# Kernel tuning notes

Measured on AMD Instinct MI355X. Metric: run time of the kernel, lower is better.

The kernel has to match this reference:

```python
import jax, jax.numpy as jnp
import numpy as np

H, I, QKV, TV = 2048, 8192, 8192, 4096
NVH, NKH, KD, VD, KC = 32, 16, 128, 128, 4

def _rms(x, w, eps=1e-6):
    # [x,-x]->LayerNorm trick: doubled mean is 0, so it reduces to x*rsqrt(mean(x^2)+eps)
    return x * jax.lax.rsqrt(jnp.mean(x * x, -1, keepdims=True) + eps) * (1.0 + w)

def _silu(x):
    return x * jax.nn.sigmoid(x)

def setup_inputs() -> dict:
    key = jax.random.key(0)
    ks = jax.random.split(key, 16)
    w = lambda i, shape, s=0.02: jax.random.normal(ks[i], shape, jnp.float32) * s
    return {
        'x': jax.random.normal(ks[0], (1, H), jnp.float32),
        'conv_state': jax.random.normal(ks[1], (QKV, KC), jnp.float32) * 0.1,
        'ssm_state': jax.random.normal(ks[2], (NVH, KD, VD), jnp.float32) * 0.1,
        'in_proj_w': w(3, (QKV + TV + 2 * NVH, H)),
        'out_proj_w': w(4, (H, TV)),
        'conv_weight': w(5, (QKV, KC), 0.5),
        'A_log': w(6, (NVH,), 0.1),
        'dt_bias': w(7, (NVH,), 0.1),
        'norm_weight': jnp.ones((VD,), jnp.float32),
        'rms1_w': w(8, (H,)),
        'rms2_w': w(9, (H,)),
        'gate_w': w(10, (I, H)),
        'up_w': w(11, (I, H)),
        'down_w': w(12, (H, I)),
    }

def reference(x, conv_state, ssm_state, in_proj_w, out_proj_w, conv_weight,
              A_log, dt_bias, norm_weight, rms1_w, rms2_w, gate_w, up_w, down_w):
    residual = x  # [1, H]
    h = _rms(x, rms1_w)
    proj = h @ in_proj_w.T  # [1, QKV+TV+2*NVH]
    mixed_qkv = proj[:, :QKV]
    z = proj[:, QKV:QKV + TV]
    a_raw = proj[0, QKV + TV:QKV + TV + NVH]
    b_raw = proj[0, QKV + TV + NVH:]

    # causal conv step: shift state, append new token, depthwise conv + silu
    new_conv_state = jnp.concatenate([conv_state[:, 1:], mixed_qkv[0][:, None]], axis=1)  # [QKV, KC]
    conv_out = _silu(jnp.sum(new_conv_state * conv_weight, axis=1))  # [QKV]

    KT = NKH * KD
    q = conv_out[:KT].reshape(NKH, KD)
    k = conv_out[KT:2 * KT].reshape(NKH, KD)
    v = conv_out[2 * KT:].reshape(NVH, VD)
    ratio = NVH // NKH
    q = jnp.repeat(q, ratio, axis=0)  # [NVH, KD]
    k = jnp.repeat(k, ratio, axis=0)
    l2 = lambda t: t / jnp.maximum(jnp.linalg.norm(t, axis=-1, keepdims=True), 1e-12)
    q = l2(q) * (KD ** -0.5)
    k = l2(k)

    beta = jax.nn.sigmoid(b_raw)  # [NVH]
    g = -jnp.exp(A_log) * jax.nn.softplus(a_raw + dt_bias)
    decay = jnp.exp(g)  # [NVH]

    # delta-rule fast-weight update
    decayed = decay[:, None, None] * ssm_state  # [NVH, KD, VD]
    Sk = jnp.einsum('hkv,hk->hv', decayed, k)
    delta = (v - Sk) * beta[:, None]
    new_ssm = decayed + k[:, :, None] * delta[:, None, :]
    y = jnp.einsum('hkv,hk->hv', new_ssm, q)  # [NVH, VD]

    # doubled-LayerNorm (eps=1e-6) with direct weight (not 1+w)
    y_n = y * jax.lax.rsqrt(jnp.mean(y * y, -1, keepdims=True) + 1e-6) * norm_weight
    y_out = (y_n * _silu(z.reshape(NVH, VD))).reshape(1, -1)  # [1, TV]
    attn_out = y_out @ out_proj_w.T
    x1 = residual + attn_out

    h2 = _rms(x1, rms2_w)
    ffn = (_silu(h2 @ gate_w.T) * (h2 @ up_w.T)) @ down_w.T
    return (x1 + ffn, new_conv_state, new_ssm)
```

## Files before the change

### kernel.cpp

```cpp
#include <hip/hip_runtime.h>
#include <math.h>

#define HD    2048
#define QKVD  8192
#define TVD   4096
#define NVHD  32
#define NKHD  16
#define KDD   128
#define VDD   128
#define PROJN (QKVD + TVD + 2*NVHD)

typedef float f4 __attribute__((ext_vector_type(4)));

__device__ __forceinline__ float sigmoidf_(float x) { return 1.0f / (1.0f + expf(-x)); }
__device__ __forceinline__ float siluf_(float x)    { return x / (1.0f + expf(-x)); }
__device__ __forceinline__ float softplusf_(float x){ return (x > 20.0f) ? x : log1pf(expf(x)); }
__device__ __forceinline__ float dot4(f4 a, f4 b)   { return a.x*b.x + a.y*b.y + a.z*b.z + a.w*b.w; }
__device__ __forceinline__ f4 ntload(const f4* p)   { return __builtin_nontemporal_load(p); }

__device__ __forceinline__ float waveReduceSum(float v) {
#pragma unroll
    for (int o = 32; o > 0; o >>= 1) v += __shfl_down(v, o, 64);
    return v;
}

template<int NW>
__device__ __forceinline__ float blockReduceSum(float v, float* red) {
    const int lane = threadIdx.x & 63, wid = threadIdx.x >> 6;
    v = waveReduceSum(v);
    if (lane == 0) red[wid] = v;
    __syncthreads();
    float s = 0.f;
#pragma unroll
    for (int w = 0; w < NW; w++) s += red[w];
    __syncthreads();
    return s;
}

__global__ void kA_inproj(const float* __restrict__ x, const float* __restrict__ w1,
                          const float* __restrict__ W, float* __restrict__ proj) {
    __shared__ float red[4];
    __shared__ float hl[HD];
    const int t = threadIdx.x;

    f4 xv[2];
    float s = 0.f;
#pragma unroll
    for (int i = 0; i < 2; i++) {
        xv[i] = ((const f4*)x)[t + i*256];
        s += dot4(xv[i], xv[i]);
    }
    s = blockReduceSum<4>(s, red);
    const float r = rsqrtf(s / (float)HD + 1e-6f);
#pragma unroll
    for (int i = 0; i < 2; i++) {
        f4 wv = ((const f4*)w1)[t + i*256];
        ((f4*)hl)[t + i*256] = xv[i] * r * (wv + 1.0f);
    }
    __syncthreads();

    const int wid = t >> 6, lane = t & 63;
    const int row = blockIdx.x * 4 + wid;
    const f4* Wr = (const f4*)(W + (size_t)row * HD);
    float acc = 0.f;
#pragma unroll
    for (int i = 0; i < 8; i++) {
        f4 a = ntload(&Wr[lane + i*64]);
        f4 b = ((const f4*)hl)[lane + i*64];
        acc += dot4(a, b);
    }
    acc = waveReduceSum(acc);
    if (lane == 0) proj[row] = acc;
}

__global__ void kB_ssm(const float* __restrict__ proj,
                       const float* __restrict__ conv_state,
                       const float* __restrict__ conv_weight,
                       const float* __restrict__ ssm_state,
                       const float* __restrict__ A_log,
                       const float* __restrict__ dt_bias,
                       const float* __restrict__ norm_weight,
                       float* __restrict__ new_conv_state,
                       float* __restrict__ new_ssm,
                       float* __restrict__ yout) {
    const int head  = blockIdx.x;
    const int t     = threadIdx.x;
    const int qhead = head >> 1;

    __shared__ float red[8];
    __shared__ float q_s[KDD], k_s[KDD], v_s[VDD];
    __shared__ float skr2[512], sqr2[512];

    float qv = 0.f, kv = 0.f, vv = 0.f;
    if (t < 128) {
        int cq = qhead*KDD + t;
        f4 cs = *(const f4*)(conv_state + (size_t)cq*4);
        f4 w  = *(const f4*)(conv_weight + (size_t)cq*4);
        float xm = proj[cq];
        qv = siluf_(cs.y*w.x + cs.z*w.y + cs.w*w.z + xm*w.w);
        f4 nc; nc.x = cs.y; nc.y = cs.z; nc.z = cs.w; nc.w = xm;
        *(f4*)(new_conv_state + (size_t)cq*4) = nc;

        int ck = 2048 + qhead*KDD + t;
        cs = *(const f4*)(conv_state + (size_t)ck*4);
        w  = *(const f4*)(conv_weight + (size_t)ck*4);
        xm = proj[ck];
        kv = siluf_(cs.y*w.x + cs.z*w.y + cs.w*w.z + xm*w.w);
        nc.x = cs.y; nc.y = cs.z; nc.z = cs.w; nc.w = xm;
        *(f4*)(new_conv_state + (size_t)ck*4) = nc;

        int cv = 4096 + head*VDD + t;
        cs = *(const f4*)(conv_state + (size_t)cv*4);
        w  = *(const f4*)(conv_weight + (size_t)cv*4);
        xm = proj[cv];
        vv = siluf_(cs.y*w.x + cs.z*w.y + cs.w*w.z + xm*w.w);
        nc.x = cs.y; nc.y = cs.z; nc.z = cs.w; nc.w = xm;
        *(f4*)(new_conv_state + (size_t)cv*4) = nc;
    }

    const float sq = blockReduceSum<8>(qv*qv, red);
    const float sk = blockReduceSum<8>(kv*kv, red);
    const float qn = qv / fmaxf(sqrtf(sq), 1e-12f) * 0.08838834764831845f;
    const float kn = kv / fmaxf(sqrtf(sk), 1e-12f);
    const float kq = blockReduceSum<8>(qn*kn, red);

    if (t < 128) { q_s[t] = qn; k_s[t] = kn; v_s[t] = vv; }
    __syncthreads();

    const float a_raw = proj[QKVD + TVD + head];
    const float b_raw = proj[QKVD + TVD + NVHD + head];
    const float beta  = sigmoidf_(b_raw);
    const float g     = -expf(A_log[head]) * softplusf_(a_raw + dt_bias[head]);
    const float decay = expf(g);

    const int col = t & 127;
    const int kh  = t >> 7;
    const float* Sp = ssm_state + (size_t)head*KDD*VDD + (size_t)kh*32*VDD + col;
    float skr = 0.f, sqr = 0.f;
#pragma unroll 8
    for (int k = 0; k < 32; k++) {
        float sv = Sp[k*VDD];
        skr += sv * k_s[kh*32 + k];
        sqr += sv * q_s[kh*32 + k];
    }
    skr2[t] = skr; sqr2[t] = sqr;
    __syncthreads();
    const float Skr = skr2[col] + skr2[col+128] + skr2[col+256] + skr2[col+384];
    const float Sqr = sqr2[col] + sqr2[col+128] + sqr2[col+256] + sqr2[col+384];
    const float delta = (v_s[col] - decay * Skr) * beta;

    float* Np = new_ssm + (size_t)head*KDD*VDD + (size_t)kh*32*VDD + col;
#pragma unroll 8
    for (int k = 0; k < 32; k++) {
        float sv = Sp[k*VDD];
        Np[k*VDD] = decay * sv + k_s[kh*32 + k] * delta;
    }

    const float y = decay * Sqr + delta * kq;
    const float sy = blockReduceSum<8>((kh == 0) ? y*y : 0.f, red);
    if (t < 128) {
        const float rr = rsqrtf(sy / (float)VDD + 1e-6f);
        const float z  = proj[QKVD + head*VDD + t];
        yout[head*VDD + t] = y * rr * norm_weight[t] * siluf_(z);
    }
}

__global__ void kC_outproj(const float* __restrict__ W, const float* __restrict__ y,
                           const float* __restrict__ x, float* __restrict__ x1) {
    __shared__ float part[4];
    const int t = threadIdx.x, wid = t >> 6, lane = t & 63;
    const int row = blockIdx.x;
    const f4* Wr = (const f4*)(W + (size_t)row * TVD);
    const f4* vr = (const f4*)y;
    float acc = 0.f;
#pragma unroll
    for (int i = 0; i < 4; i++) {
        int idx = wid*256 + i*64 + lane;
        acc += dot4(ntload(&Wr[idx]), vr[idx]);
    }
    acc = waveReduceSum(acc);
    if (lane == 0) part[wid] = acc;
    __syncthreads();
    if (t == 0) x1[row] = x[row] + part[0] + part[1] + part[2] + part[3];
}

__global__ void kD_gateup(const float* __restrict__ GW, const float* __restrict__ UW,
                          const float* __restrict__ x1, const float* __restrict__ w2,
                          float* __restrict__ m) {
    __shared__ float red[4];
    __shared__ float tl[HD];
    const int t = threadIdx.x;

    f4 xv[2];
    float s = 0.f;
#pragma unroll
    for (int i = 0; i < 2; i++) {
        xv[i] = ((const f4*)x1)[t + i*256];
        s += dot4(xv[i], xv[i]);
    }
    s = blockReduceSum<4>(s, red);
    const float r = rsqrtf(s / (float)HD + 1e-6f);
#pragma unroll
    for (int i = 0; i < 2; i++) {
        f4 wv = ((const f4*)w2)[t + i*256];
        ((f4*)tl)[t + i*256] = xv[i] * (wv + 1.0f);
    }
    __syncthreads();

    const int wid = t >> 6, lane = t & 63;
    const int row = blockIdx.x * 4 + wid;
    const f4* Gr = (const f4*)(GW + (size_t)row * HD);
    const f4* Ur = (const f4*)(UW + (size_t)row * HD);
    float ag = 0.f, au = 0.f;
#pragma unroll
    for (int i = 0; i < 8; i++) {
        f4 tt = ((const f4*)tl)[lane + i*64];
        ag += dot4(ntload(&Gr[lane + i*64]), tt);
        au += dot4(ntload(&Ur[lane + i*64]), tt);
    }
    ag = waveReduceSum(ag);
    au = waveReduceSum(au);
    if (lane == 0) {
        ag *= r; au *= r;
        m[row] = siluf_(ag) * au;
    }
}

__global__ void kE_down(const float* __restrict__ W, const float* __restrict__ m,
                        const float* __restrict__ x1, float* __restrict__ out0) {
    __shared__ float part[4];
    const int t = threadIdx.x, wid = t >> 6, lane = t & 63;
    const int row = blockIdx.x;
    const f4* Wr = (const f4*)(W + (size_t)row * 8192);
    const f4* vr = (const f4*)m;
    float acc = 0.f;
#pragma unroll
    for (int i = 0; i < 8; i++) {
        int idx = wid*512 + i*64 + lane;
        acc += dot4(ntload(&Wr[idx]), vr[idx]);
    }
    acc = waveReduceSum(acc);
    if (lane == 0) part[wid] = acc;
    __syncthreads();
    if (t == 0) out0[row] = x1[row] + part[0] + part[1] + part[2] + part[3];
}

extern "C" void kernel_launch(void* const* d_in, const int* in_sizes, int n_in,
                              void* d_out, int out_size, void* d_ws, size_t ws_size,
                              hipStream_t stream) {
    const float* x           = (const float*)d_in[0];
    const float* conv_state  = (const float*)d_in[1];
    const float* ssm_state   = (const float*)d_in[2];
    const float* in_proj_w   = (const float*)d_in[3];
    const float* out_proj_w  = (const float*)d_in[4];
    const float* conv_weight = (const float*)d_in[5];
    const float* A_log       = (const float*)d_in[6];
    const float* dt_bias     = (const float*)d_in[7];
    const float* norm_weight = (const float*)d_in[8];
    const float* rms1_w      = (const float*)d_in[9];
    const float* rms2_w      = (const float*)d_in[10];
    const float* gate_w      = (const float*)d_in[11];
    const float* up_w        = (const float*)d_in[12];
    const float* down_w      = (const float*)d_in[13];

    float* out0     = (float*)d_out;
    float* new_conv = out0 + HD;
    float* new_ssm  = new_conv + QKVD*4;

    float* ws   = (float*)d_ws;
    float* proj = ws;
    float* yout = proj + PROJN;
    float* x1   = yout + TVD;
    float* mmid = x1 + HD;

    kA_inproj<<<PROJN/4, 256, 0, stream>>>(x, rms1_w, in_proj_w, proj);
    kB_ssm<<<NVHD, 512, 0, stream>>>(proj, conv_state, conv_weight, ssm_state,
                                     A_log, dt_bias, norm_weight,
                                     new_conv, new_ssm, yout);
    kC_outproj<<<HD, 256, 0, stream>>>(out_proj_w, yout, x, x1);
    kD_gateup<<<8192/4, 256, 0, stream>>>(gate_w, up_w, x1, rms2_w, mmid);
    kE_down<<<HD, 256, 0, stream>>>(down_w, mmid, x1, out0);
}
```

Before: 311.3 us.

## Remove shared-memory staging and block syncs from GEMV kernels; one row per wave

The in-projection and gate/up kernels now have each wave compute the RMS-norm scale and the normalized input vector in registers, instead of staging them in shared memory behind block-wide barriers. The RMS scale is applied to the final dot product rather than to the input. The out-proj and down-proj kernels switch from four waves sharing one row (shared-memory partial sums plus a barrier) to one row per wave, with a quarter as many blocks. This drops barriers and LDS traffic, but the small input vector is now re-read per wave and each wave streams a longer row.

```diff
diff --git a/kernel.cpp b/kernel.cpp
--- a/kernel.cpp
+++ b/kernel.cpp
@@ -5,7 +5,6 @@
 #define QKVD  8192
 #define TVD   4096
 #define NVHD  32
-#define NKHD  16
 #define KDD   128
 #define VDD   128
 #define PROJN (QKVD + TVD + 2*NVHD)
@@ -39,38 +38,26 @@
 
 __global__ void kA_inproj(const float* __restrict__ x, const float* __restrict__ w1,
                           const float* __restrict__ W, float* __restrict__ proj) {
-    __shared__ float red[4];
-    __shared__ float hl[HD];
-    const int t = threadIdx.x;
-
-    f4 xv[2];
-    float s = 0.f;
-#pragma unroll
-    for (int i = 0; i < 2; i++) {
-        xv[i] = ((const f4*)x)[t + i*256];
-        s += dot4(xv[i], xv[i]);
-    }
-    s = blockReduceSum<4>(s, red);
-    const float r = rsqrtf(s / (float)HD + 1e-6f);
-#pragma unroll
-    for (int i = 0; i < 2; i++) {
-        f4 wv = ((const f4*)w1)[t + i*256];
-        ((f4*)hl)[t + i*256] = xv[i] * r * (wv + 1.0f);
-    }
-    __syncthreads();
-
-    const int wid = t >> 6, lane = t & 63;
-    const int row = blockIdx.x * 4 + wid;
+    const int t = threadIdx.x, wid = t >> 6, lane = t & 63;
+    const int row = blockIdx.x * 4 + wid;
+
+    f4 tt[8];
+    float ss = 0.f;
+#pragma unroll
+    for (int i = 0; i < 8; i++) {
+        f4 xv = ((const f4*)x)[lane + i*64];
+        f4 wv = ((const f4*)w1)[lane + i*64];
+        ss += dot4(xv, xv);
+        tt[i] = xv * (wv + 1.0f);
+    }
     const f4* Wr = (const f4*)(W + (size_t)row * HD);
     float acc = 0.f;
 #pragma unroll
-    for (int i = 0; i < 8; i++) {
-        f4 a = ntload(&Wr[lane + i*64]);
-        f4 b = ((const f4*)hl)[lane + i*64];
-        acc += dot4(a, b);
-    }
+    for (int i = 0; i < 8; i++)
+        acc += dot4(ntload(&Wr[lane + i*64]), tt[i]);
     acc = waveReduceSum(acc);
-    if (lane == 0) proj[row] = acc;
+    ss  = waveReduceSum(ss);
+    if (lane == 0) proj[row] = acc * rsqrtf(ss / (float)HD + 1e-6f);
 }
 
 __global__ void kB_ssm(const float* __restrict__ proj,
@@ -167,82 +154,62 @@
 
 __global__ void kC_outproj(const float* __restrict__ W, const float* __restrict__ y,
                            const float* __restrict__ x, float* __restrict__ x1) {
-    __shared__ float part[4];
-    const int t = threadIdx.x, wid = t >> 6, lane = t & 63;
-    const int row = blockIdx.x;
+    const int t = threadIdx.x, wid = t >> 6, lane = t & 63;
+    const int row = blockIdx.x * 4 + wid;
     const f4* Wr = (const f4*)(W + (size_t)row * TVD);
     const f4* vr = (const f4*)y;
     float acc = 0.f;
-#pragma unroll
-    for (int i = 0; i < 4; i++) {
-        int idx = wid*256 + i*64 + lane;
-        acc += dot4(ntload(&Wr[idx]), vr[idx]);
-    }
+#pragma unroll 8
+    for (int i = 0; i < 16; i++)
+        acc += dot4(ntload(&Wr[lane + i*64]), vr[lane + i*64]);
     acc = waveReduceSum(acc);
-    if (lane == 0) part[wid] = acc;
-    __syncthreads();
-    if (t == 0) x1[row] = x[row] + part[0] + part[1] + part[2] + part[3];
+    if (lane == 0) x1[row] = x[row] + acc;
 }
 
 __global__ void kD_gateup(const float* __restrict__ GW, const float* __restrict__ UW,
                           const float* __restrict__ x1, const float* __restrict__ w2,
                           float* __restrict__ m) {
-    __shared__ float red[4];
-    __shared__ float tl[HD];
-    const int t = threadIdx.x;
-
-    f4 xv[2];
-    float s = 0.f;
-#pragma unroll
-    for (int i = 0; i < 2; i++) {
-        xv[i] = ((const f4*)x1)[t + i*256];
-        s += dot4(xv[i], xv[i]);
-    }
-    s = blockReduceSum<4>(s, red);
-    const float r = rsqrtf(s / (float)HD + 1e-6f);
-#pragma unroll
-    for (int i = 0; i < 2; i++) {
-        f4 wv = ((const f4*)w2)[t + i*256];
-        ((f4*)tl)[t + i*256] = xv[i] * (wv + 1.0f);
-    }
-    __syncthreads();
-
-    const int wid = t >> 6, lane = t & 63;
-    const int row = blockIdx.x * 4 + wid;
+    const int t = threadIdx.x, wid = t >> 6, lane = t & 63;
+    const int row = blockIdx.x * 4 + wid;
+
+    f4 tt[8];
+    float ss = 0.f;
+#pragma unroll
+    for (int i = 0; i < 8; i++) {
+        f4 xv = ((const f4*)x1)[lane + i*64];
+        f4 wv = ((const f4*)w2)[lane + i*64];
+        ss += dot4(xv, xv);
+        tt[i] = xv * (wv + 1.0f);
+    }
     const f4* Gr = (const f4*)(GW + (size_t)row * HD);
     const f4* Ur = (const f4*)(UW + (size_t)row * HD);
     float ag = 0.f, au = 0.f;
-#pragma unroll
+#pragma unroll 4
     for (int i = 0; i < 8; i++) {
-        f4 tt = ((const f4*)tl)[lane + i*64];
-        ag += dot4(ntload(&Gr[lane + i*64]), tt);
-        au += dot4(ntload(&Ur[lane + i*64]), tt);
+        ag += dot4(ntload(&Gr[lane + i*64]), tt[i]);
+        au += dot4(ntload(&Ur[lane + i*64]), tt[i]);
     }
     ag = waveReduceSum(ag);
     au = waveReduceSum(au);
+    ss = waveReduceSum(ss);
     if (lane == 0) {
-        ag *= r; au *= r;
-        m[row] = siluf_(ag) * au;
+        const float r = rsqrtf(ss / (float)HD + 1e-6f);
+        m[row] = siluf_(ag * r) * (au * r);
     }
 }
 
 __global__ void kE_down(const float* __restrict__ W, const float* __restrict__ m,
                         const float* __restrict__ x1, float* __restrict__ out0) {
-    __shared__ float part[4];
-    const int t = threadIdx.x, wid = t >> 6, lane = t & 63;
-    const int row = blockIdx.x;
+    const int t = threadIdx.x, wid = t >> 6, lane = t & 63;
+    const int row = blockIdx.x * 4 + wid;
     const f4* Wr = (const f4*)(W + (size_t)row * 8192);
     const f4* vr = (const f4*)m;
     float acc = 0.f;
-#pragma unroll
-    for (int i = 0; i < 8; i++) {
-        int idx = wid*512 + i*64 + lane;
-        acc += dot4(ntload(&Wr[idx]), vr[idx]);
-    }
+#pragma unroll 8
+    for (int i = 0; i < 32; i++)
+        acc += dot4(ntload(&Wr[lane + i*64]), vr[lane + i*64]);
     acc = waveReduceSum(acc);
-    if (lane == 0) part[wid] = acc;
-    __syncthreads();
-    if (t == 0) out0[row] = x1[row] + part[0] + part[1] + part[2] + part[3];
+    if (lane == 0) out0[row] = x1[row] + acc;
 }
 
 extern "C" void kernel_launch(void* const* d_in, const int* in_sizes, int n_in,
@@ -277,7 +244,7 @@
     kB_ssm<<<NVHD, 512, 0, stream>>>(proj, conv_state, conv_weight, ssm_state,
                                      A_log, dt_bias, norm_weight,
                                      new_conv, new_ssm, yout);
-    kC_outproj<<<HD, 256, 0, stream>>>(out_proj_w, yout, x, x1);
+    kC_outproj<<<HD/4, 256, 0, stream>>>(out_proj_w, yout, x, x1);
     kD_gateup<<<8192/4, 256, 0, stream>>>(gate_w, up_w, x1, rms2_w, mmid);
-    kE_down<<<HD, 256, 0, stream>>>(down_w, mmid, x1, out0);
-}
+    kE_down<<<HD/4, 256, 0, stream>>>(down_w, mmid, x1, out0);
+}
```

Measured after the change: 322.8 us. +3.7%, slower.

## Fuse all stages into one persistent kernel with grid barriers

Applied to the files above, without the earlier changes.

Replaces the five separate kernel launches with one persistent 128-block kernel that moves between stages through atomic grid barriers, removing launch gaps and tail idle time. While 32 blocks run the SSM head update, the other blocks pre-read the out-projection weights to warm the cache for the next stage. The out-projection now uses cached loads instead of nontemporal ones. The risks are fewer blocks in flight to saturate HBM bandwidth for the large GEMVs, barrier spin overhead, and a hang if all 128 blocks are not co-resident.

```diff
diff --git a/kernel.cpp b/kernel.cpp
--- a/kernel.cpp
+++ b/kernel.cpp
@@ -5,10 +5,11 @@
 #define QKVD  8192
 #define TVD   4096
 #define NVHD  32
-#define NKHD  16
 #define KDD   128
 #define VDD   128
 #define PROJN (QKVD + TVD + 2*NVHD)
+#define NB    128
+#define BT    256
 
 typedef float f4 __attribute__((ext_vector_type(4)));
 
@@ -37,212 +38,220 @@
     return s;
 }
 
-__global__ void kA_inproj(const float* __restrict__ x, const float* __restrict__ w1,
-                          const float* __restrict__ W, float* __restrict__ proj) {
+__device__ __forceinline__ void gridBar(int* bar, int idx) {
+    __syncthreads();
+    __threadfence();
+    if (threadIdx.x == 0) {
+        __hip_atomic_fetch_add(&bar[idx], 1, __ATOMIC_ACQ_REL, __HIP_MEMORY_SCOPE_AGENT);
+        while (__hip_atomic_load(&bar[idx], __ATOMIC_ACQUIRE, __HIP_MEMORY_SCOPE_AGENT) < NB)
+            __builtin_amdgcn_s_sleep(8);
+    }
+    __syncthreads();
+    __threadfence();
+}
+
+__global__ void init_bar(int* bar) {
+    if (threadIdx.x < 8) bar[threadIdx.x] = 0;
+}
+
+__global__ __launch_bounds__(BT)
+void mega(const float* __restrict__ x, const float* __restrict__ conv_state,
+          const float* __restrict__ ssm_state, const float* __restrict__ in_proj_w,
+          const float* __restrict__ out_proj_w, const float* __restrict__ conv_weight,
+          const float* __restrict__ A_log, const float* __restrict__ dt_bias,
+          const float* __restrict__ norm_weight, const float* __restrict__ rms1_w,
+          const float* __restrict__ rms2_w, const float* __restrict__ gate_w,
+          const float* __restrict__ up_w, const float* __restrict__ down_w,
+          float* __restrict__ out0, float* __restrict__ new_conv,
+          float* __restrict__ new_ssm, float* __restrict__ proj,
+          float* __restrict__ yout, float* __restrict__ x1, float* __restrict__ mmid,
+          int* __restrict__ bar) {
+    __shared__ float hl[HD];
     __shared__ float red[4];
-    __shared__ float hl[HD];
-    const int t = threadIdx.x;
-
-    f4 xv[2];
-    float s = 0.f;
-#pragma unroll
-    for (int i = 0; i < 2; i++) {
-        xv[i] = ((const f4*)x)[t + i*256];
-        s += dot4(xv[i], xv[i]);
-    }
-    s = blockReduceSum<4>(s, red);
-    const float r = rsqrtf(s / (float)HD + 1e-6f);
-#pragma unroll
-    for (int i = 0; i < 2; i++) {
-        f4 wv = ((const f4*)w1)[t + i*256];
-        ((f4*)hl)[t + i*256] = xv[i] * r * (wv + 1.0f);
-    }
-    __syncthreads();
-
+    __shared__ float q_s[KDD], k_s[KDD], v_s[VDD];
+    __shared__ float skr2[256], sqr2[256];
+    const int t = threadIdx.x, bid = blockIdx.x;
     const int wid = t >> 6, lane = t & 63;
-    const int row = blockIdx.x * 4 + wid;
-    const f4* Wr = (const f4*)(W + (size_t)row * HD);
-    float acc = 0.f;
-#pragma unroll
-    for (int i = 0; i < 8; i++) {
-        f4 a = ntload(&Wr[lane + i*64]);
-        f4 b = ((const f4*)hl)[lane + i*64];
-        acc += dot4(a, b);
-    }
-    acc = waveReduceSum(acc);
-    if (lane == 0) proj[row] = acc;
-}
-
-__global__ void kB_ssm(const float* __restrict__ proj,
-                       const float* __restrict__ conv_state,
-                       const float* __restrict__ conv_weight,
-                       const float* __restrict__ ssm_state,
-                       const float* __restrict__ A_log,
-                       const float* __restrict__ dt_bias,
-                       const float* __restrict__ norm_weight,
-                       float* __restrict__ new_conv_state,
-                       float* __restrict__ new_ssm,
-                       float* __restrict__ yout) {
-    const int head  = blockIdx.x;
-    const int t     = threadIdx.x;
-    const int qhead = head >> 1;
-
-    __shared__ float red[8];
-    __shared__ float q_s[KDD], k_s[KDD], v_s[VDD];
-    __shared__ float skr2[512], sqr2[512];
-
-    float qv = 0.f, kv = 0.f, vv = 0.f;
-    if (t < 128) {
-        int cq = qhead*KDD + t;
-        f4 cs = *(const f4*)(conv_state + (size_t)cq*4);
-        f4 w  = *(const f4*)(conv_weight + (size_t)cq*4);
-        float xm = proj[cq];
-        qv = siluf_(cs.y*w.x + cs.z*w.y + cs.w*w.z + xm*w.w);
-        f4 nc; nc.x = cs.y; nc.y = cs.z; nc.z = cs.w; nc.w = xm;
-        *(f4*)(new_conv_state + (size_t)cq*4) = nc;
-
-        int ck = 2048 + qhead*KDD + t;
-        cs = *(const f4*)(conv_state + (size_t)ck*4);
-        w  = *(const f4*)(conv_weight + (size_t)ck*4);
-        xm = proj[ck];
-        kv = siluf_(cs.y*w.x + cs.z*w.y + cs.w*w.z + xm*w.w);
-        nc.x = cs.y; nc.y = cs.z; nc.z = cs.w; nc.w = xm;
-        *(f4*)(new_conv_state + (size_t)ck*4) = nc;
-
-        int cv = 4096 + head*VDD + t;
-        cs = *(const f4*)(conv_state + (size_t)cv*4);
-        w  = *(const f4*)(conv_weight + (size_t)cv*4);
-        xm = proj[cv];
-        vv = siluf_(cs.y*w.x + cs.z*w.y + cs.w*w.z + xm*w.w);
-        nc.x = cs.y; nc.y = cs.z; nc.z = cs.w; nc.w = xm;
-        *(f4*)(new_conv_state + (size_t)cv*4) = nc;
-    }
-
-    const float sq = blockReduceSum<8>(qv*qv, red);
-    const float sk = blockReduceSum<8>(kv*kv, red);
-    const float qn = qv / fmaxf(sqrtf(sq), 1e-12f) * 0.08838834764831845f;
-    const float kn = kv / fmaxf(sqrtf(sk), 1e-12f);
-    const float kq = blockReduceSum<8>(qn*kn, red);
-
-    if (t < 128) { q_s[t] = qn; k_s[t] = kn; v_s[t] = vv; }
-    __syncthreads();
-
-    const float a_raw = proj[QKVD + TVD + head];
-    const float b_raw = proj[QKVD + TVD + NVHD + head];
-    const float beta  = sigmoidf_(b_raw);
-    const float g     = -expf(A_log[head]) * softplusf_(a_raw + dt_bias[head]);
-    const float decay = expf(g);
-
-    const int col = t & 127;
-    const int kh  = t >> 7;
-    const float* Sp = ssm_state + (size_t)head*KDD*VDD + (size_t)kh*32*VDD + col;
-    float skr = 0.f, sqr = 0.f;
+
+    {
+        f4 xv[2];
+        float s = 0.f;
+#pragma unroll
+        for (int i = 0; i < 2; i++) {
+            xv[i] = ((const f4*)x)[t + i*256];
+            s += dot4(xv[i], xv[i]);
+        }
+        s = blockReduceSum<4>(s, red);
+        const float r = rsqrtf(s / (float)HD + 1e-6f);
+#pragma unroll
+        for (int i = 0; i < 2; i++) {
+            f4 wv = ((const f4*)rms1_w)[t + i*256];
+            ((f4*)hl)[t + i*256] = xv[i] * r * (wv + 1.0f);
+        }
+        __syncthreads();
+    }
+
+    for (int row = bid*4 + wid; row < PROJN; row += NB*4) {
+        const f4* Wr = (const f4*)(in_proj_w + (size_t)row * HD);
+        float acc = 0.f;
+#pragma unroll
+        for (int i = 0; i < 8; i++)
+            acc += dot4(ntload(&Wr[lane + i*64]), ((const f4*)hl)[lane + i*64]);
+        acc = waveReduceSum(acc);
+        if (lane == 0) proj[row] = acc;
+    }
+    gridBar(bar, 0);
+
+    if (bid < NVHD) {
+        const int head = bid, qhead = head >> 1;
+        float qv = 0.f, kv = 0.f, vv = 0.f;
+        if (t < 128) {
+            int cq = qhead*KDD + t;
+            f4 cs = *(const f4*)(conv_state + (size_t)cq*4);
+            f4 w  = *(const f4*)(conv_weight + (size_t)cq*4);
+            float xm = proj[cq];
+            qv = siluf_(cs.y*w.x + cs.z*w.y + cs.w*w.z + xm*w.w);
+            f4 nc; nc.x = cs.y; nc.y = cs.z; nc.z = cs.w; nc.w = xm;
+            *(f4*)(new_conv + (size_t)cq*4) = nc;
+
+            int ck = 2048 + qhead*KDD + t;
+            cs = *(const f4*)(conv_state + (size_t)ck*4);
+            w  = *(const f4*)(conv_weight + (size_t)ck*4);
+            xm = proj[ck];
+            kv = siluf_(cs.y*w.x + cs.z*w.y + cs.w*w.z + xm*w.w);
+            nc.x = cs.y; nc.y = cs.z; nc.z = cs.w; nc.w = xm;
+            *(f4*)(new_conv + (size_t)ck*4) = nc;
+
+            int cv = 4096 + head*VDD + t;
+            cs = *(const f4*)(conv_state + (size_t)cv*4);
+            w  = *(const f4*)(conv_weight + (size_t)cv*4);
+            xm = proj[cv];
+            vv = siluf_(cs.y*w.x + cs.z*w.y + cs.w*w.z + xm*w.w);
+            nc.x = cs.y; nc.y = cs.z; nc.z = cs.w; nc.w = xm;
+            *(f4*)(new_conv + (size_t)cv*4) = nc;
+        }
+
+        const float sq = blockReduceSum<4>(qv*qv, red);
+        const float sk = blockReduceSum<4>(kv*kv, red);
+        const float qn = qv / fmaxf(sqrtf(sq), 1e-12f) * 0.08838834764831845f;
+        const float kn = kv / fmaxf(sqrtf(sk), 1e-12f);
+        const float kq = blockReduceSum<4>(qn*kn, red);
+
+        if (t < 128) { q_s[t] = qn; k_s[t] = kn; v_s[t] = vv; }
+        __syncthreads();
+
+        const float a_raw = proj[QKVD + TVD + head];
+        const float b_raw = proj[QKVD + TVD + NVHD + head];
+        const float beta  = sigmoidf_(b_raw);
+        const float g     = -expf(A_log[head]) * softplusf_(a_raw + dt_bias[head]);
+        const float decay = expf(g);
+
+        const int col = t & 127;
+        const int kh  = t >> 7;
+        const float* Sp = ssm_state + (size_t)head*KDD*VDD + (size_t)kh*64*VDD + col;
+        float skr = 0.f, sqr = 0.f;
+#pragma unroll 16
+        for (int k = 0; k < 64; k++) {
+            float sv = Sp[k*VDD];
+            skr += sv * k_s[kh*64 + k];
+            sqr += sv * q_s[kh*64 + k];
+        }
+        skr2[t] = skr; sqr2[t] = sqr;
+        __syncthreads();
+        const float Skr = skr2[col] + skr2[col + 128];
+        const float Sqr = sqr2[col] + sqr2[col + 128];
+        const float delta = (v_s[col] - decay * Skr) * beta;
+
+        float* Np = new_ssm + (size_t)head*KDD*VDD + (size_t)kh*64*VDD + col;
+#pragma unroll 16
+        for (int k = 0; k < 64; k++) {
+            float sv = Sp[k*VDD];
+            Np[k*VDD] = decay * sv + k_s[kh*64 + k] * delta;
+        }
+
+        const float y = decay * Sqr + delta * kq;
+        const float sy = blockReduceSum<4>((kh == 0) ? y*y : 0.f, red);
+        if (t < 128) {
+            const float rr = rsqrtf(sy / (float)VDD + 1e-6f);
+            const float z  = proj[QKVD + head*VDD + t];
+            yout[head*VDD + t] = y * rr * norm_weight[t] * siluf_(z);
+        }
+    } else {
+        const f4* P = (const f4*)out_proj_w;
+        const int n = HD*TVD/4;
+        float acc = 0.f;
+        for (int i = (bid - NVHD)*BT + t; i < n; i += (NB - NVHD)*BT) {
+            f4 v = P[i];
+            acc += v.x + v.y + v.z + v.w;
+        }
+        asm volatile("" :: "v"(acc));
+    }
+    gridBar(bar, 1);
+
+    {
+#pragma unroll
+        for (int rr = 0; rr < 4; rr++) {
+            const int row = bid*4 + wid + rr*(NB*4);
+            const f4* Wr = (const f4*)(out_proj_w + (size_t)row * TVD);
+            const f4* vr = (const f4*)yout;
+            float acc = 0.f;
+#pragma unroll
+            for (int i = 0; i < 16; i++)
+                acc += dot4(Wr[lane + i*64], vr[lane + i*64]);
+            acc = waveReduceSum(acc);
+            if (lane == 0) x1[row] = x[row] + acc;
+        }
+    }
+    gridBar(bar, 2);
+
+    {
+        f4 yv[2];
+        float s = 0.f;
+#pragma unroll
+        for (int i = 0; i < 2; i++) {
+            yv[i] = ((const f4*)x1)[t + i*256];
+            s += dot4(yv[i], yv[i]);
+        }
+        s = blockReduceSum<4>(s, red);
+        const float r = rsqrtf(s / (float)HD + 1e-6f);
+#pragma unroll
+        for (int i = 0; i < 2; i++) {
+            f4 wv = ((const f4*)rms2_w)[t + i*256];
+            ((f4*)hl)[t + i*256] = yv[i] * (wv + 1.0f);
+        }
+        __syncthreads();
+
+        for (int row = bid*4 + wid; row < 8192; row += NB*4) {
+            const f4* Gr = (const f4*)(gate_w + (size_t)row * HD);
+            const f4* Ur = (const f4*)(up_w   + (size_t)row * HD);
+            float ag = 0.f, au = 0.f;
+#pragma unroll
+            for (int i = 0; i < 8; i++) {
+                f4 tt = ((const f4*)hl)[lane + i*64];
+                ag += dot4(ntload(&Gr[lane + i*64]), tt);
+                au += dot4(ntload(&Ur[lane + i*64]), tt);
+            }
+            ag = waveReduceSum(ag);
+            au = waveReduceSum(au);
+            if (lane == 0) mmid[row] = siluf_(ag * r) * (au * r);
+        }
+    }
+    gridBar(bar, 3);
+
+    {
+#pragma unroll
+        for (int rr = 0; rr < 4; rr++) {
+            const int row = bid*4 + wid + rr*(NB*4);
+            const f4* Wr = (const f4*)(down_w + (size_t)row * 8192);
+            const f4* vr = (const f4*)mmid;
+            float acc = 0.f;
 #pragma unroll 8
-    for (int k = 0; k < 32; k++) {
-        float sv = Sp[k*VDD];
-        skr += sv * k_s[kh*32 + k];
-        sqr += sv * q_s[kh*32 + k];
-    }
-    skr2[t] = skr; sqr2[t] = sqr;
-    __syncthreads();
-    const float Skr = skr2[col] + skr2[col+128] + skr2[col+256] + skr2[col+384];
-    const float Sqr = sqr2[col] + sqr2[col+128] + sqr2[col+256] + sqr2[col+384];
-    const float delta = (v_s[col] - decay * Skr) * beta;
-
-    float* Np = new_ssm + (size_t)head*KDD*VDD + (size_t)kh*32*VDD + col;
-#pragma unroll 8
-    for (int k = 0; k < 32; k++) {
-        float sv = Sp[k*VDD];
-        Np[k*VDD] = decay * sv + k_s[kh*32 + k] * delta;
-    }
-
-    const float y = decay * Sqr + delta * kq;
-    const float sy = blockReduceSum<8>((kh == 0) ? y*y : 0.f, red);
-    if (t < 128) {
-        const float rr = rsqrtf(sy / (float)VDD + 1e-6f);
-        const float z  = proj[QKVD + head*VDD + t];
-        yout[head*VDD + t] = y * rr * norm_weight[t] * siluf_(z);
-    }
-}
-
-__global__ void kC_outproj(const float* __restrict__ W, const float* __restrict__ y,
-                           const float* __restrict__ x, float* __restrict__ x1) {
-    __shared__ float part[4];
-    const int t = threadIdx.x, wid = t >> 6, lane = t & 63;
-    const int row = blockIdx.x;
-    const f4* Wr = (const f4*)(W + (size_t)row * TVD);
-    const f4* vr = (const f4*)y;
-    float acc = 0.f;
-#pragma unroll
-    for (int i = 0; i < 4; i++) {
-        int idx = wid*256 + i*64 + lane;
-        acc += dot4(ntload(&Wr[idx]), vr[idx]);
-    }
-    acc = waveReduceSum(acc);
-    if (lane == 0) part[wid] = acc;
-    __syncthreads();
-    if (t == 0) x1[row] = x[row] + part[0] + part[1] + part[2] + part[3];
-}
-
-__global__ void kD_gateup(const float* __restrict__ GW, const float* __restrict__ UW,
-                          const float* __restrict__ x1, const float* __restrict__ w2,
-                          float* __restrict__ m) {
-    __shared__ float red[4];
-    __shared__ float tl[HD];
-    const int t = threadIdx.x;
-
-    f4 xv[2];
-    float s = 0.f;
-#pragma unroll
-    for (int i = 0; i < 2; i++) {
-        xv[i] = ((const f4*)x1)[t + i*256];
-        s += dot4(xv[i], xv[i]);
-    }
-    s = blockReduceSum<4>(s, red);
-    const float r = rsqrtf(s / (float)HD + 1e-6f);
-#pragma unroll
-    for (int i = 0; i < 2; i++) {
-        f4 wv = ((const f4*)w2)[t + i*256];
-        ((f4*)tl)[t + i*256] = xv[i] * (wv + 1.0f);
-    }
-    __syncthreads();
-
-    const int wid = t >> 6, lane = t & 63;
-    const int row = blockIdx.x * 4 + wid;
-    const f4* Gr = (const f4*)(GW + (size_t)row * HD);
-    const f4* Ur = (const f4*)(UW + (size_t)row * HD);
-    float ag = 0.f, au = 0.f;
-#pragma unroll
-    for (int i = 0; i < 8; i++) {
-        f4 tt = ((const f4*)tl)[lane + i*64];
-        ag += dot4(ntload(&Gr[lane + i*64]), tt);
-        au += dot4(ntload(&Ur[lane + i*64]), tt);
-    }
-    ag = waveReduceSum(ag);
-    au = waveReduceSum(au);
-    if (lane == 0) {
-        ag *= r; au *= r;
-        m[row] = siluf_(ag) * au;
-    }
-}
-
-__global__ void kE_down(const float* __restrict__ W, const float* __restrict__ m,
-                        const float* __restrict__ x1, float* __restrict__ out0) {
-    __shared__ float part[4];
-    const int t = threadIdx.x, wid = t >> 6, lane = t & 63;
-    const int row = blockIdx.x;
-    const f4* Wr = (const f4*)(W + (size_t)row * 8192);
-    const f4* vr = (const f4*)m;
-    float acc = 0.f;
-#pragma unroll
-    for (int i = 0; i < 8; i++) {
-        int idx = wid*512 + i*64 + lane;
-        acc += dot4(ntload(&Wr[idx]), vr[idx]);
-    }
-    acc = waveReduceSum(acc);
-    if (lane == 0) part[wid] = acc;
-    __syncthreads();
-    if (t == 0) out0[row] = x1[row] + part[0] + part[1] + part[2] + part[3];
+            for (int i = 0; i < 32; i++)
+                acc += dot4(ntload(&Wr[lane + i*64]), vr[lane + i*64]);
+            acc = waveReduceSum(acc);
+            if (lane == 0) out0[row] = x1[row] + acc;
+        }
+    }
 }
 
 extern "C" void kernel_launch(void* const* d_in, const int* in_sizes, int n_in,
@@ -272,12 +281,11 @@
     float* yout = proj + PROJN;
     float* x1   = yout + TVD;
     float* mmid = x1 + HD;
-
-    kA_inproj<<<PROJN/4, 256, 0, stream>>>(x, rms1_w, in_proj_w, proj);
-    kB_ssm<<<NVHD, 512, 0, stream>>>(proj, conv_state, conv_weight, ssm_state,
-                                     A_log, dt_bias, norm_weight,
-                                     new_conv, new_ssm, yout);
-    kC_outproj<<<HD, 256, 0, stream>>>(out_proj_w, yout, x, x1);
-    kD_gateup<<<8192/4, 256, 0, stream>>>(gate_w, up_w, x1, rms2_w, mmid);
-    kE_down<<<HD, 256, 0, stream>>>(down_w, mmid, x1, out0);
-}
+    int*   bar  = (int*)(mmid + 8192);
+
+    init_bar<<<1, 64, 0, stream>>>(bar);
+    mega<<<NB, BT, 0, stream>>>(x, conv_state, ssm_state, in_proj_w, out_proj_w,
+                                conv_weight, A_log, dt_bias, norm_weight,
+                                rms1_w, rms2_w, gate_w, up_w, down_w,
+                                out0, new_conv, new_ssm, proj, yout, x1, mmid, bar);
+}
```

After: 458.1 us. +47.2%, slower.
